# Optimization experiments

Hardware: AMD Instinct MI355X
Metric: run time of the kernel (lower is better)

Reference implementation:

```python
import jax, jax.numpy as jnp
import numpy as np

H = 64          # heightmap size (sqrt of in_channels=4096)
FEATS = [8, 16, 32, 64]
NEG_SLOPE = 0.01
EPS = 1e-12


def setup_inputs() -> dict:
    key = jax.random.key(0)
    ks = jax.random.split(key, 32)
    inp = {"x": jax.random.normal(ks[0], (16384, H * H), dtype=jnp.float32)}
    in_feat = H
    ki = 1
    for li, out_feat in enumerate(FEATS):
        bound = np.sqrt(6.0 / (in_feat + out_feat))  # xavier_uniform
        inp[f"w{li}"] = jax.random.uniform(ks[ki], (out_feat, in_feat), minval=-bound, maxval=bound, dtype=jnp.float32); ki += 1
        inp[f"b{li}"] = jnp.zeros((out_feat,), dtype=jnp.float32)
        inp[f"s{li}"] = jnp.ones((1,), dtype=jnp.float32)  # sigma parameter
        in_feat = out_feat
    compress_in = H * FEATS[-1]
    inp["wm0"] = jax.random.normal(ks[ki], (80, compress_in), dtype=jnp.float32) * 0.02; ki += 1
    inp["bm0"] = jnp.zeros((80,), dtype=jnp.float32)
    inp["wm1"] = jax.random.normal(ks[ki], (60, 80), dtype=jnp.float32) * 0.02; ki += 1
    inp["bm1"] = jnp.zeros((60,), dtype=jnp.float32)
    return inp


def _gauss_layer(x, dist_sq, sigma, w, b):
    # x: [B, H, Cin] ; dist_sq: [H, H] ; w: [Cout, Cin]
    xp = jnp.einsum('bhc,oc->bho', x, w) + b
    k = jnp.exp(-dist_sq / (2.0 * sigma[0] ** 2))                 # [H, H]
    k = k / jnp.maximum(jnp.sum(k, axis=-1, keepdims=True), EPS)  # L1 normalize
    out = jnp.einsum('ij,bjc->bic', k, xp)
    return jax.nn.leaky_relu(out, NEG_SLOPE)


def reference(x, w0, b0, s0, w1, b1, s1, w2, b2, s2, w3, b3, s3, wm0, bm0, wm1, bm1):
    B = x.shape[0]
    h = x.reshape(B, H, H)
    idx = jnp.arange(H, dtype=x.dtype)
    dist_sq = (idx[:, None] - idx[None, :]) ** 2  # coords are 1-D row indices
    for sigma, w, b in ((s0, w0, b0), (s1, w1, b1), (s2, w2, b2), (s3, w3, b3)):
        h = _gauss_layer(h, dist_sq, sigma, w, b)
    h = h.reshape(B, -1)                              # [B, H*64]
    h = jax.nn.leaky_relu(h @ wm0.T + bm0, NEG_SLOPE)
    h = jax.nn.leaky_relu(h @ wm1.T + bm1, NEG_SLOPE)
    return h
```

## Files before the change

### kernel.cpp

```cpp
#include <hip/hip_runtime.h>


typedef _Float16 f16x8 __attribute__((ext_vector_type(8)));
typedef _Float16 f16x4 __attribute__((ext_vector_type(4)));
typedef float    f32x4 __attribute__((ext_vector_type(4)));

#define KT_OFF    327680
#define W0P_OFF   344064
#define W1P_OFF   345088
#define W2P_OFF   345600
#define W3P_OFF   346624
#define H_BYTE_OFF 1048576

__global__ void prep_all(const float* __restrict__ s0, const float* __restrict__ s1,
                         const float* __restrict__ s2, const float* __restrict__ s3,
                         const float* __restrict__ w0, const float* __restrict__ w1,
                         const float* __restrict__ w2, const float* __restrict__ w3,
                         const float* __restrict__ wm0, _Float16* __restrict__ base) {
  int bid = blockIdx.x, tid = threadIdx.x;
  if (bid < 1280) {
    int idx = bid * 256 + tid;
    int kc = idx / 2560, rem = idx % 2560;
    int n = rem >> 5, o = rem & 31;
    base[idx] = (_Float16)wm0[n * 4096 + kc * 32 + o];
  } else if (bid == 1280) {
    int li = tid >> 6, i = tid & 63;
    float sg = (li == 0) ? s0[0] : (li == 1) ? s1[0] : (li == 2) ? s2[0] : s3[0];
    float denom = 2.0f * sg * sg;
    float sum = 0.0f;
    for (int j = 0; j < 64; ++j) {
      float d = (float)(i - j);
      sum += expf(-(d * d) / denom);
    }
    float inv = 1.0f / fmaxf(sum, 1e-12f);
    for (int j = 0; j < 64; ++j) {
      float d = (float)(i - j);
      base[KT_OFF + (li * 64 + i) * 64 + j] = (_Float16)(expf(-(d * d) / denom) * inv);
    }
  } else {
    for (int r = tid; r < 4608; r += 256) {
      float v;
      if (r < 1024)      { int o = r >> 6, c = r & 63;             v = (o < 8)  ? w0[o * 64 + c] : 0.0f; }
      else if (r < 1536) { int q = r - 1024; int o = q >> 5, c = q & 31; v = (c < 8)  ? w1[o * 8 + c]  : 0.0f; }
      else if (r < 2560) { int q = r - 1536; int o = q >> 5, c = q & 31; v = (c < 16) ? w2[o * 16 + c] : 0.0f; }
      else               { int q = r - 2560; int o = q >> 5, c = q & 31; v = w3[o * 32 + c]; }
      base[W0P_OFF + r] = (_Float16)v;
    }
  }
}

__device__ __forceinline__ float leaky(float v) { return v > 0.0f ? v : 0.01f * v; }

__device__ __forceinline__ int swz(int row, int c) {
  return row * 64 + ((((c >> 3) ^ (row & 7))) << 3) + (c & 7);
}

template<int NT, int KC, int KPAD>
__device__ __forceinline__ void stage_a(_Float16* __restrict__ P,
                                        const _Float16* __restrict__ wp, const float* bv,
                                        int lo, int hi) {
  f16x8 a[4][KC];
#pragma unroll
  for (int mt = 0; mt < 4; ++mt)
#pragma unroll
    for (int kc = 0; kc < KC; ++kc)
      a[mt][kc] = *(const f16x8*)(P + swz(mt * 16 + lo, kc * 32 + hi * 8));
  f16x8 wf[NT][KC];
#pragma unroll
  for (int nt = 0; nt < NT; ++nt)
#pragma unroll
    for (int kc = 0; kc < KC; ++kc)
      wf[nt][kc] = *(const f16x8*)(wp + (nt * 16 + lo) * KPAD + kc * 32 + hi * 8);
#pragma unroll
  for (int mt = 0; mt < 4; ++mt)
#pragma unroll
    for (int nt = 0; nt < NT; ++nt) {
      f32x4 acc = {0.0f, 0.0f, 0.0f, 0.0f};
#pragma unroll
      for (int kc = 0; kc < KC; ++kc)
        acc = __builtin_amdgcn_mfma_f32_16x16x32_f16(a[mt][kc], wf[nt][kc], acc, 0, 0, 0);
      f16x4 hv;
#pragma unroll
      for (int r = 0; r < 4; ++r) hv[r] = (_Float16)(acc[r] + bv[nt]);
      *(f16x4*)(P + swz(nt * 16 + lo, mt * 16 + hi * 4)) = hv;
    }
}

template<int MT>
__device__ __forceinline__ void stage_b(_Float16* __restrict__ P,
                                        const _Float16* __restrict__ kmat, int lo, int hi) {
  f16x8 ax[MT][2];
#pragma unroll
  for (int ot = 0; ot < MT; ++ot)
#pragma unroll
    for (int kc = 0; kc < 2; ++kc)
      ax[ot][kc] = *(const f16x8*)(P + swz(ot * 16 + lo, kc * 32 + hi * 8));
  f16x8 kb[4][2];
#pragma unroll
  for (int nt = 0; nt < 4; ++nt)
#pragma unroll
    for (int kc = 0; kc < 2; ++kc)
      kb[nt][kc] = *(const f16x8*)(kmat + (nt * 16 + lo) * 64 + kc * 32 + hi * 8);
#pragma unroll
  for (int ot = 0; ot < MT; ++ot)
#pragma unroll
    for (int nt = 0; nt < 4; ++nt) {
      f32x4 acc = {0.0f, 0.0f, 0.0f, 0.0f};
#pragma unroll
      for (int kc = 0; kc < 2; ++kc)
        acc = __builtin_amdgcn_mfma_f32_16x16x32_f16(ax[ot][kc], kb[nt][kc], acc, 0, 0, 0);
      f16x4 hv;
#pragma unroll
      for (int r = 0; r < 4; ++r) hv[r] = (_Float16)leaky(acc[r]);
      *(f16x4*)(P + swz(nt * 16 + lo, ot * 16 + hi * 4)) = hv;
    }
}

__global__ __launch_bounds__(256, 4)
void gauss_phase(const float* __restrict__ x, _Float16* __restrict__ hout,
                 const float* __restrict__ bb0, const float* __restrict__ bb1,
                 const float* __restrict__ bb2, const float* __restrict__ bb3,
                 const _Float16* __restrict__ wsh, int B) {
  __shared__ _Float16 lds[4][4096];
  const int tid = threadIdx.x;
  const int wv = tid >> 6, lane = tid & 63;
  const int lo = lane & 15, hi = lane >> 4;
  const int smp = blockIdx.x * 4 + wv;
  if (smp >= B) return;
  _Float16* P = lds[wv];

  float bv0 = (lo < 8) ? bb0[lo] : 0.0f;
  float bv1 = bb1[lo];
  float bv2[2] = {bb2[lo], bb2[16 + lo]};
  float bv3[4] = {bb3[lo], bb3[16 + lo], bb3[32 + lo], bb3[48 + lo]};

  const float4* xv = (const float4*)(x + (size_t)smp * 4096);
#pragma unroll
  for (int t = 0; t < 16; ++t) {
    float4 v = xv[t * 64 + lane];
    f16x4 hv;
    hv[0] = (_Float16)v.x; hv[1] = (_Float16)v.y; hv[2] = (_Float16)v.z; hv[3] = (_Float16)v.w;
    *(f16x4*)(P + swz(t * 4 + hi, lo * 4)) = hv;
  }

  const _Float16* kt = wsh + KT_OFF;
  stage_a<1, 2, 64>(P, wsh + W0P_OFF, &bv0, lo, hi);
  stage_b<1>(P, kt + 0 * 4096, lo, hi);
  stage_a<1, 1, 32>(P, wsh + W1P_OFF, &bv1, lo, hi);
  stage_b<1>(P, kt + 1 * 4096, lo, hi);
  stage_a<2, 1, 32>(P, wsh + W2P_OFF, bv2, lo, hi);
  stage_b<2>(P, kt + 2 * 4096, lo, hi);
  stage_a<4, 1, 32>(P, wsh + W3P_OFF, bv3, lo, hi);
  stage_b<4>(P, kt + 3 * 4096, lo, hi);

  _Float16* g = hout + (size_t)blockIdx.x * 16384 + wv * 32 + (lane & 3) * 8;
#pragma unroll
  for (int t = 0; t < 8; ++t) {
    int c = t * 64 + lane;
    int i = c >> 3, j = c & 7;
    f16x8 v = *(const f16x8*)(P + i * 64 + ((j ^ (i & 7)) << 3));
    *(f16x8*)(g + (size_t)(t * 16 + (lane >> 2)) * 128) = v;
  }
}

__global__ __launch_bounds__(256, 4)
void dense_phase(const _Float16* __restrict__ h, const _Float16* __restrict__ wm0t,
                 const float* __restrict__ bm0, const float* __restrict__ wm1,
                 const float* __restrict__ bm1, float* __restrict__ out, int B) {
  __shared__ float part[4][16][84];
  __shared__ float h1[16][84];
  const int tid = threadIdx.x;
  const int wv = tid >> 6, lane = tid & 63;
  const int lo = lane & 15, hi = lane >> 4;
  const int m0 = blockIdx.x * 16;

  int smp = m0 + lo;
  if (smp >= B) smp = B - 1;
  const _Float16* abase = h + (size_t)(smp >> 2) * 16384 + (smp & 3) * 32 + hi * 8;
  const _Float16* bbase = wm0t + (size_t)lo * 32 + hi * 8;

  f32x4 acc[5];
#pragma unroll
  for (int nt = 0; nt < 5; ++nt) { f32x4 z = {0.0f, 0.0f, 0.0f, 0.0f}; acc[nt] = z; }

#pragma unroll 2
  for (int it = 0; it < 32; ++it) {
    int kc = wv * 32 + it;
    f16x8 a = *(const f16x8*)(abase + (size_t)kc * 128);
    const _Float16* bp = bbase + (size_t)kc * 2560;
#pragma unroll
    for (int nt = 0; nt < 5; ++nt) {
      f16x8 b = *(const f16x8*)(bp + nt * 512);
      acc[nt] = __builtin_amdgcn_mfma_f32_16x16x32_f16(a, b, acc[nt], 0, 0, 0);
    }
  }
#pragma unroll
  for (int nt = 0; nt < 5; ++nt)
#pragma unroll
    for (int r = 0; r < 4; ++r)
      part[wv][hi * 4 + r][nt * 16 + lo] = acc[nt][r];
  __syncthreads();

  for (int e = tid; e < 16 * 80; e += 256) {
    int m = e / 80, n = e - m * 80;
    float v = bm0[n] + part[0][m][n] + part[1][m][n] + part[2][m][n] + part[3][m][n];
    h1[m][n] = leaky(v);
  }
  __syncthreads();

  for (int e = tid; e < 16 * 60; e += 256) {
    int m = e / 60, n = e - m * 60;
    float v = bm1[n];
    const float4* hr = (const float4*)&h1[m][0];
    const float4* wr = (const float4*)(wm1 + n * 80);
#pragma unroll
    for (int k2 = 0; k2 < 20; ++k2) {
      float4 hv = hr[k2], wv4 = wr[k2];
      v += hv.x * wv4.x + hv.y * wv4.y + hv.z * wv4.z + hv.w * wv4.w;
    }
    int s = m0 + m;
    if (s < B) out[(size_t)s * 60 + n] = leaky(v);
  }
}

extern "C" void kernel_launch(void* const* d_in, const int* in_sizes, int n_in,
                              void* d_out, int out_size, void* d_ws, size_t ws_size,
                              hipStream_t stream) {
  const float* x   = (const float*)d_in[0];
  const float* w0  = (const float*)d_in[1];
  const float* b0  = (const float*)d_in[2];
  const float* s0  = (const float*)d_in[3];
  const float* w1  = (const float*)d_in[4];
  const float* b1  = (const float*)d_in[5];
  const float* s1  = (const float*)d_in[6];
  const float* w2  = (const float*)d_in[7];
  const float* b2  = (const float*)d_in[8];
  const float* s2  = (const float*)d_in[9];
  const float* w3  = (const float*)d_in[10];
  const float* b3  = (const float*)d_in[11];
  const float* s3  = (const float*)d_in[12];
  const float* wm0 = (const float*)d_in[13];
  const float* bm0 = (const float*)d_in[14];
  const float* wm1 = (const float*)d_in[15];
  const float* bm1 = (const float*)d_in[16];
  float* out = (float*)d_out;
  _Float16* wsh = (_Float16*)d_ws;

  int B = in_sizes[0] / 4096;
  size_t h_need = H_BYTE_OFF + (size_t)B * 4096 * 2;
  _Float16* hbuf = (ws_size >= h_need) ? (_Float16*)((char*)d_ws + H_BYTE_OFF)
                                       : (_Float16*)const_cast<float*>(x);

  prep_all<<<1282, 256, 0, stream>>>(s0, s1, s2, s3, w0, w1, w2, w3, wm0, wsh);
  gauss_phase<<<(B + 3) / 4, 256, 0, stream>>>(x, hbuf, b0, b1, b2, b3, wsh, B);
  dense_phase<<<(B + 15) / 16, 256, 0, stream>>>(hbuf, wsh, bm0, wm1, bm1, out, B);
}
```

Measured before the change: 190.9 us.

## Fuse gaussian layers and dense MLP into one kernel keeping activations in LDS

Merges the gaussian-layer kernel and the dense-layer kernel into a single 512-thread kernel that handles 8 samples per block. The final 64x64 activations stay in LDS and feed the wm0 MFMA directly, so the fp16 intermediate buffer is never written to or read back from global memory. The swizzle now folds in a per-wave XOR so the dense stage can read eight samples' LDS regions without bank conflicts. In exchange, only 8 of the 16 MFMA rows carry real samples, so half the dense-stage MFMA work is wasted and block size and LDS use go up.

```diff
diff --git a/kernel.cpp b/kernel.cpp
--- a/kernel.cpp
+++ b/kernel.cpp
@@ -10,7 +10,6 @@
 #define W1P_OFF   345088
 #define W2P_OFF   345600
 #define W3P_OFF   346624
-#define H_BYTE_OFF 1048576
 
 __global__ void prep_all(const float* __restrict__ s0, const float* __restrict__ s1,
                          const float* __restrict__ s2, const float* __restrict__ s3,
@@ -51,12 +50,12 @@
 
 __device__ __forceinline__ float leaky(float v) { return v > 0.0f ? v : 0.01f * v; }
 
-__device__ __forceinline__ int swz(int row, int c) {
-  return row * 64 + ((((c >> 3) ^ (row & 7))) << 3) + (c & 7);
+__device__ __forceinline__ int swz(int sx, int row, int c) {
+  return row * 64 + ((((c >> 3) ^ (row & 7) ^ sx) & 7) << 3) + (c & 7);
 }
 
 template<int NT, int KC, int KPAD>
-__device__ __forceinline__ void stage_a(_Float16* __restrict__ P,
+__device__ __forceinline__ void stage_a(_Float16* __restrict__ P, int sx,
                                         const _Float16* __restrict__ wp, const float* bv,
                                         int lo, int hi) {
   f16x8 a[4][KC];
@@ -64,7 +63,7 @@
   for (int mt = 0; mt < 4; ++mt)
 #pragma unroll
     for (int kc = 0; kc < KC; ++kc)
-      a[mt][kc] = *(const f16x8*)(P + swz(mt * 16 + lo, kc * 32 + hi * 8));
+      a[mt][kc] = *(const f16x8*)(P + swz(sx, mt * 16 + lo, kc * 32 + hi * 8));
   f16x8 wf[NT][KC];
 #pragma unroll
   for (int nt = 0; nt < NT; ++nt)
@@ -82,19 +81,19 @@
       f16x4 hv;
 #pragma unroll
       for (int r = 0; r < 4; ++r) hv[r] = (_Float16)(acc[r] + bv[nt]);
-      *(f16x4*)(P + swz(nt * 16 + lo, mt * 16 + hi * 4)) = hv;
+      *(f16x4*)(P + swz(sx, nt * 16 + lo, mt * 16 + hi * 4)) = hv;
     }
 }
 
 template<int MT>
-__device__ __forceinline__ void stage_b(_Float16* __restrict__ P,
+__device__ __forceinline__ void stage_b(_Float16* __restrict__ P, int sx,
                                         const _Float16* __restrict__ kmat, int lo, int hi) {
   f16x8 ax[MT][2];
 #pragma unroll
   for (int ot = 0; ot < MT; ++ot)
 #pragma unroll
     for (int kc = 0; kc < 2; ++kc)
-      ax[ot][kc] = *(const f16x8*)(P + swz(ot * 16 + lo, kc * 32 + hi * 8));
+      ax[ot][kc] = *(const f16x8*)(P + swz(sx, ot * 16 + lo, kc * 32 + hi * 8));
   f16x8 kb[4][2];
 #pragma unroll
   for (int nt = 0; nt < 4; ++nt)
@@ -112,22 +111,26 @@
       f16x4 hv;
 #pragma unroll
       for (int r = 0; r < 4; ++r) hv[r] = (_Float16)leaky(acc[r]);
-      *(f16x4*)(P + swz(nt * 16 + lo, ot * 16 + hi * 4)) = hv;
-    }
-}
-
-__global__ __launch_bounds__(256, 4)
-void gauss_phase(const float* __restrict__ x, _Float16* __restrict__ hout,
-                 const float* __restrict__ bb0, const float* __restrict__ bb1,
-                 const float* __restrict__ bb2, const float* __restrict__ bb3,
-                 const _Float16* __restrict__ wsh, int B) {
-  __shared__ _Float16 lds[4][4096];
+      *(f16x4*)(P + swz(sx, nt * 16 + lo, ot * 16 + hi * 4)) = hv;
+    }
+}
+
+__global__ __launch_bounds__(512, 4)
+void fused(const float* __restrict__ x,
+           const float* __restrict__ bb0, const float* __restrict__ bb1,
+           const float* __restrict__ bb2, const float* __restrict__ bb3,
+           const _Float16* __restrict__ wsh,
+           const float* __restrict__ bm0, const float* __restrict__ wm1,
+           const float* __restrict__ bm1, float* __restrict__ out, int B) {
+  __shared__ _Float16 lds[8][4096];
   const int tid = threadIdx.x;
   const int wv = tid >> 6, lane = tid & 63;
   const int lo = lane & 15, hi = lane >> 4;
-  const int smp = blockIdx.x * 4 + wv;
-  if (smp >= B) return;
+  const int smp0 = blockIdx.x * 8;
+  int smp = smp0 + wv;
+  if (smp >= B) smp = B - 1;
   _Float16* P = lds[wv];
+  const int sx = wv;
 
   float bv0 = (lo < 8) ? bb0[lo] : 0.0f;
   float bv1 = bb1[lo];
@@ -140,85 +143,71 @@
     float4 v = xv[t * 64 + lane];
     f16x4 hv;
     hv[0] = (_Float16)v.x; hv[1] = (_Float16)v.y; hv[2] = (_Float16)v.z; hv[3] = (_Float16)v.w;
-    *(f16x4*)(P + swz(t * 4 + hi, lo * 4)) = hv;
+    *(f16x4*)(P + swz(sx, t * 4 + hi, lo * 4)) = hv;
   }
 
   const _Float16* kt = wsh + KT_OFF;
-  stage_a<1, 2, 64>(P, wsh + W0P_OFF, &bv0, lo, hi);
-  stage_b<1>(P, kt + 0 * 4096, lo, hi);
-  stage_a<1, 1, 32>(P, wsh + W1P_OFF, &bv1, lo, hi);
-  stage_b<1>(P, kt + 1 * 4096, lo, hi);
-  stage_a<2, 1, 32>(P, wsh + W2P_OFF, bv2, lo, hi);
-  stage_b<2>(P, kt + 2 * 4096, lo, hi);
-  stage_a<4, 1, 32>(P, wsh + W3P_OFF, bv3, lo, hi);
-  stage_b<4>(P, kt + 3 * 4096, lo, hi);
-
-  _Float16* g = hout + (size_t)blockIdx.x * 16384 + wv * 32 + (lane & 3) * 8;
-#pragma unroll
-  for (int t = 0; t < 8; ++t) {
-    int c = t * 64 + lane;
-    int i = c >> 3, j = c & 7;
-    f16x8 v = *(const f16x8*)(P + i * 64 + ((j ^ (i & 7)) << 3));
-    *(f16x8*)(g + (size_t)(t * 16 + (lane >> 2)) * 128) = v;
-  }
-}
-
-__global__ __launch_bounds__(256, 4)
-void dense_phase(const _Float16* __restrict__ h, const _Float16* __restrict__ wm0t,
-                 const float* __restrict__ bm0, const float* __restrict__ wm1,
-                 const float* __restrict__ bm1, float* __restrict__ out, int B) {
-  __shared__ float part[4][16][84];
-  __shared__ float h1[16][84];
-  const int tid = threadIdx.x;
-  const int wv = tid >> 6, lane = tid & 63;
-  const int lo = lane & 15, hi = lane >> 4;
-  const int m0 = blockIdx.x * 16;
-
-  int smp = m0 + lo;
-  if (smp >= B) smp = B - 1;
-  const _Float16* abase = h + (size_t)(smp >> 2) * 16384 + (smp & 3) * 32 + hi * 8;
-  const _Float16* bbase = wm0t + (size_t)lo * 32 + hi * 8;
+  stage_a<1, 2, 64>(P, sx, wsh + W0P_OFF, &bv0, lo, hi);
+  stage_b<1>(P, sx, kt + 0 * 4096, lo, hi);
+  stage_a<1, 1, 32>(P, sx, wsh + W1P_OFF, &bv1, lo, hi);
+  stage_b<1>(P, sx, kt + 1 * 4096, lo, hi);
+  stage_a<2, 1, 32>(P, sx, wsh + W2P_OFF, bv2, lo, hi);
+  stage_b<2>(P, sx, kt + 2 * 4096, lo, hi);
+  stage_a<4, 1, 32>(P, sx, wsh + W3P_OFF, bv3, lo, hi);
+  stage_b<4>(P, sx, kt + 3 * 4096, lo, hi);
+
+  __syncthreads();
 
   f32x4 acc[5];
 #pragma unroll
   for (int nt = 0; nt < 5; ++nt) { f32x4 z = {0.0f, 0.0f, 0.0f, 0.0f}; acc[nt] = z; }
 
+  const _Float16* ap = &lds[lo & 7][0];
 #pragma unroll 2
-  for (int it = 0; it < 32; ++it) {
-    int kc = wv * 32 + it;
-    f16x8 a = *(const f16x8*)(abase + (size_t)kc * 128);
-    const _Float16* bp = bbase + (size_t)kc * 2560;
+  for (int it = 0; it < 16; ++it) {
+    int kc = wv * 16 + it;
+    int row = kc >> 1, cc = (kc & 1) * 32 + hi * 8;
+    f16x8 a = *(const f16x8*)(ap + swz(lo & 7, row, cc));
+    const _Float16* bp = wsh + (size_t)kc * 2560 + lo * 32 + hi * 8;
 #pragma unroll
     for (int nt = 0; nt < 5; ++nt) {
       f16x8 b = *(const f16x8*)(bp + nt * 512);
       acc[nt] = __builtin_amdgcn_mfma_f32_16x16x32_f16(a, b, acc[nt], 0, 0, 0);
     }
   }
-#pragma unroll
-  for (int nt = 0; nt < 5; ++nt)
-#pragma unroll
-    for (int r = 0; r < 4; ++r)
-      part[wv][hi * 4 + r][nt * 16 + lo] = acc[nt][r];
-  __syncthreads();
-
-  for (int e = tid; e < 16 * 80; e += 256) {
+  __syncthreads();
+
+  float* scr = (float*)&lds[0][0];
+  if (hi < 2) {
+#pragma unroll
+    for (int nt = 0; nt < 5; ++nt)
+#pragma unroll
+      for (int r = 0; r < 4; ++r)
+        scr[wv * 640 + (hi * 4 + r) * 80 + nt * 16 + lo] = acc[nt][r];
+  }
+  __syncthreads();
+
+  float* h1 = scr + 5120;
+  for (int e = tid; e < 640; e += 512) {
     int m = e / 80, n = e - m * 80;
-    float v = bm0[n] + part[0][m][n] + part[1][m][n] + part[2][m][n] + part[3][m][n];
-    h1[m][n] = leaky(v);
-  }
-  __syncthreads();
-
-  for (int e = tid; e < 16 * 60; e += 256) {
-    int m = e / 60, n = e - m * 60;
+    float v = bm0[n];
+#pragma unroll
+    for (int w = 0; w < 8; ++w) v += scr[w * 640 + e];
+    h1[e] = leaky(v);
+  }
+  __syncthreads();
+
+  if (tid < 480) {
+    int m = tid / 60, n = tid - m * 60;
     float v = bm1[n];
-    const float4* hr = (const float4*)&h1[m][0];
+    const float4* hr = (const float4*)(h1 + m * 80);
     const float4* wr = (const float4*)(wm1 + n * 80);
 #pragma unroll
     for (int k2 = 0; k2 < 20; ++k2) {
       float4 hv = hr[k2], wv4 = wr[k2];
       v += hv.x * wv4.x + hv.y * wv4.y + hv.z * wv4.z + hv.w * wv4.w;
     }
-    int s = m0 + m;
+    int s = smp0 + m;
     if (s < B) out[(size_t)s * 60 + n] = leaky(v);
   }
 }
@@ -247,11 +236,7 @@
   _Float16* wsh = (_Float16*)d_ws;
 
   int B = in_sizes[0] / 4096;
-  size_t h_need = H_BYTE_OFF + (size_t)B * 4096 * 2;
-  _Float16* hbuf = (ws_size >= h_need) ? (_Float16*)((char*)d_ws + H_BYTE_OFF)
-                                       : (_Float16*)const_cast<float*>(x);
 
   prep_all<<<1282, 256, 0, stream>>>(s0, s1, s2, s3, w0, w1, w2, w3, wm0, wsh);
-  gauss_phase<<<(B + 3) / 4, 256, 0, stream>>>(x, hbuf, b0, b1, b2, b3, wsh, B);
-  dense_phase<<<(B + 15) / 16, 256, 0, stream>>>(hbuf, wsh, bm0, wm1, bm1, out, B);
-}
+  fused<<<(B + 7) / 8, 512, 0, stream>>>(x, b0, b1, b2, b3, wsh, bm0, wm1, bm1, out, B);
+}
```

Result: no change. 189.0 us (-1.0%).
